# Kernel tuning notes

Hardware: AMD Instinct MI355X
Metric: run time of the kernel (lower is better)

The kernel has to match this reference:

```python
import jax, jax.numpy as jnp
import numpy as np

SQRT_2_OVER_PI = 0.7978845608028654
GELU_COEFF = 0.044715

def _gelu_tanh(v):
    inner = SQRT_2_OVER_PI * (v + GELU_COEFF * v * v * v)
    return 0.5 * v * (1.0 + jnp.tanh(inner))

def setup_inputs() -> dict:
    key = jax.random.key(0)
    k1, k2, k3, k4 = jax.random.split(key, 4)
    M, K, N = 16384, 4096, 4096
    x = jax.random.normal(k1, (M, K), dtype=jnp.float32)
    bound_w = np.sqrt(6.0 / K) / np.sqrt(1.0 + 5.0)  # kaiming_uniform a=sqrt(5)
    weight = jax.random.uniform(k2, (K, N), dtype=jnp.float32, minval=-bound_w, maxval=bound_w)
    bound_b = 1.0 / np.sqrt(K)
    bias = jax.random.uniform(k3, (N,), dtype=jnp.float32, minval=-bound_b, maxval=bound_b)
    subtract = jax.random.normal(k4, (N,), dtype=jnp.float32)
    return {"x": x, "weight": weight, "bias": bias, "subtract": subtract}

def reference(x, weight, bias, subtract):
    # mean_n(xW + b - s) = (x . colsum(W) + sum(b) - sum(s)) / N
    N = weight.shape[1]
    c = weight.sum(axis=1)                       # (K,)
    scale = 1.0 / N
    bias_term = (bias.sum() - subtract.sum()) * scale
    row_scalars = _gelu_tanh(x @ c * scale + bias_term)  # (M,)
    return x + row_scalars[:, None]
```

## Files before the change

kernel.cpp:

```cpp
#include <hip/hip_runtime.h>
#include <math.h>

#define K_DIM 4096
#define N_DIM 4096

typedef float f32x4 __attribute__((ext_vector_type(4)));

__global__ void __launch_bounds__(256) colsum_kernel(const float* __restrict__ W,
                                                     const float* __restrict__ bias,
                                                     const float* __restrict__ subtract,
                                                     float* __restrict__ c,
                                                     float* __restrict__ bterm) {
    const int t = threadIdx.x;
    __shared__ float s[4];
    const int wave = t >> 6, lane = t & 63;

    if (blockIdx.x < K_DIM) {
        const int k = blockIdx.x;
        const f32x4* row = reinterpret_cast<const f32x4*>(W + (size_t)k * N_DIM);
        float acc = 0.f;
#pragma unroll
        for (int i = 0; i < N_DIM / 4 / 256; ++i) {
            f32x4 v = __builtin_nontemporal_load(&row[t + i * 256]);
            acc += (v.x + v.y) + (v.z + v.w);
        }
#pragma unroll
        for (int off = 32; off > 0; off >>= 1) acc += __shfl_down(acc, off, 64);
        if (lane == 0) s[wave] = acc;
        __syncthreads();
        if (t == 0) c[k] = (s[0] + s[1]) + (s[2] + s[3]);
    } else {
        float acc = 0.f;
        for (int i = t; i < N_DIM; i += 256) acc += bias[i] - subtract[i];
#pragma unroll
        for (int off = 32; off > 0; off >>= 1) acc += __shfl_down(acc, off, 64);
        if (lane == 0) s[wave] = acc;
        __syncthreads();
        if (t == 0) bterm[0] = ((s[0] + s[1]) + (s[2] + s[3])) * (1.0f / (float)N_DIM);
    }
}


#define PROCESS(XV, ROFF)                                                        \
    do {                                                                         \
        float a0 = 0.f, a1 = 0.f, a2 = 0.f, a3 = 0.f;                            \
        _Pragma("unroll")                                                        \
        for (int i = 0; i < 16; ++i) {                                           \
            f32x4 cvv = c4[lane + i * 64];                                       \
            a0 += XV[i].x * cvv.x;                                               \
            a1 += XV[i].y * cvv.y;                                               \
            a2 += XV[i].z * cvv.z;                                               \
            a3 += XV[i].w * cvv.w;                                               \
        }                                                                        \
        float acc = (a0 + a1) + (a2 + a3);                                       \
        _Pragma("unroll")                                                        \
        for (int off = 32; off > 0; off >>= 1) acc += __shfl_xor(acc, off, 64);  \
        float d = acc * (1.0f / (float)N_DIM) + bt;                              \
        float inner = 0.7978845608028654f * (d + 0.044715f * d * d * d);         \
        float e  = __expf(2.0f * inner);                                         \
        float g  = 0.5f * d * (1.0f + (1.0f - 2.0f / (e + 1.0f)));               \
        _Pragma("unroll")                                                        \
        for (int i = 0; i < 16; ++i) {                                           \
            f32x4 o = XV[i] + g;                                                 \
            __builtin_nontemporal_store(o, &orow[(size_t)(ROFF) * 1024 + lane + i * 64]); \
        }                                                                        \
    } while (0)

__global__ void __launch_bounds__(256) rowfuse_kernel(const float* __restrict__ x,
                                                      const float* __restrict__ c,
                                                      const float* __restrict__ bterm,
                                                      float* __restrict__ out) {
    const int t = threadIdx.x;
    const int wave = t >> 6, lane = t & 63;
    const size_t w = (size_t)blockIdx.x * 4 + wave;

    const f32x4* c4 = reinterpret_cast<const f32x4*>(c);
    const f32x4* xr = reinterpret_cast<const f32x4*>(x) + w * 4 * (K_DIM / 4);
    f32x4* orow     = reinterpret_cast<f32x4*>(out)     + w * 4 * (K_DIM / 4);
    const float bt = bterm[0];

    f32x4 xa[16], xb[16];
#pragma unroll
    for (int i = 0; i < 16; ++i) xa[i] = __builtin_nontemporal_load(&xr[lane + i * 64]);

#pragma unroll
    for (int i = 0; i < 16; ++i) xb[i] = __builtin_nontemporal_load(&xr[1024 + lane + i * 64]);
    PROCESS(xa, 0);

#pragma unroll
    for (int i = 0; i < 16; ++i) xa[i] = __builtin_nontemporal_load(&xr[2048 + lane + i * 64]);
    PROCESS(xb, 1);

#pragma unroll
    for (int i = 0; i < 16; ++i) xb[i] = __builtin_nontemporal_load(&xr[3072 + lane + i * 64]);
    PROCESS(xa, 2);

    PROCESS(xb, 3);
}

extern "C" void kernel_launch(void* const* d_in, const int* in_sizes, int n_in,
                              void* d_out, int out_size, void* d_ws, size_t ws_size,
                              hipStream_t stream) {
    const float* x        = (const float*)d_in[0];
    const float* W        = (const float*)d_in[1];
    const float* bias     = (const float*)d_in[2];
    const float* subtract = (const float*)d_in[3];
    float* out = (float*)d_out;

    float* c     = (float*)d_ws;
    float* bterm = c + K_DIM;

    const int M = in_sizes[0] / K_DIM;

    colsum_kernel<<<K_DIM + 1, 256, 0, stream>>>(W, bias, subtract, c, bterm);
    rowfuse_kernel<<<M / 16, 256, 0, stream>>>(x, c, bterm, out);
}
```

Before: 114.8 us.

## Fuse column-sum and row GELU kernels into one cooperative grid-synced kernel

Replaces the two launches with a single cooperative kernel. Each wave first sums two rows of W into c and preloads its first x row, then the grid synchronizes before each wave processes eight rows of x in a double-buffered pipeline. The aim is to remove the second launch and the gap between kernels, and to overlap the W reduction with the x prefetch. The cost is a grid-wide barrier, plus the requirement that all 256 blocks of 512 threads are co-resident under launch_bounds(512,2) with 32 f32x4 registers per thread.

```diff
diff --git a/kernel.cpp b/kernel.cpp
--- a/kernel.cpp
+++ b/kernel.cpp
@@ -1,4 +1,5 @@
 #include <hip/hip_runtime.h>
+#include <hip/hip_cooperative_groups.h>
 #include <math.h>
 
 #define K_DIM 4096
@@ -6,40 +7,7 @@
 
 typedef float f32x4 __attribute__((ext_vector_type(4)));
 
-__global__ void __launch_bounds__(256) colsum_kernel(const float* __restrict__ W,
-                                                     const float* __restrict__ bias,
-                                                     const float* __restrict__ subtract,
-                                                     float* __restrict__ c,
-                                                     float* __restrict__ bterm) {
-    const int t = threadIdx.x;
-    __shared__ float s[4];
-    const int wave = t >> 6, lane = t & 63;
-
-    if (blockIdx.x < K_DIM) {
-        const int k = blockIdx.x;
-        const f32x4* row = reinterpret_cast<const f32x4*>(W + (size_t)k * N_DIM);
-        float acc = 0.f;
-#pragma unroll
-        for (int i = 0; i < N_DIM / 4 / 256; ++i) {
-            f32x4 v = __builtin_nontemporal_load(&row[t + i * 256]);
-            acc += (v.x + v.y) + (v.z + v.w);
-        }
-#pragma unroll
-        for (int off = 32; off > 0; off >>= 1) acc += __shfl_down(acc, off, 64);
-        if (lane == 0) s[wave] = acc;
-        __syncthreads();
-        if (t == 0) c[k] = (s[0] + s[1]) + (s[2] + s[3]);
-    } else {
-        float acc = 0.f;
-        for (int i = t; i < N_DIM; i += 256) acc += bias[i] - subtract[i];
-#pragma unroll
-        for (int off = 32; off > 0; off >>= 1) acc += __shfl_down(acc, off, 64);
-        if (lane == 0) s[wave] = acc;
-        __syncthreads();
-        if (t == 0) bterm[0] = ((s[0] + s[1]) + (s[2] + s[3])) * (1.0f / (float)N_DIM);
-    }
-}
-
+namespace cg = cooperative_groups;
 
 #define PROCESS(XV, ROFF)                                                        \
     do {                                                                         \
@@ -62,40 +30,78 @@
         _Pragma("unroll")                                                        \
         for (int i = 0; i < 16; ++i) {                                           \
             f32x4 o = XV[i] + g;                                                 \
-            __builtin_nontemporal_store(o, &orow[(size_t)(ROFF) * 1024 + lane + i * 64]); \
+            __builtin_nontemporal_store(o, &o4[(size_t)(ROFF) * 1024 + lane + i * 64]); \
         }                                                                        \
     } while (0)
 
-__global__ void __launch_bounds__(256) rowfuse_kernel(const float* __restrict__ x,
-                                                      const float* __restrict__ c,
-                                                      const float* __restrict__ bterm,
-                                                      float* __restrict__ out) {
+#define LOADB(BUF, R)                                                            \
+    do {                                                                         \
+        _Pragma("unroll")                                                        \
+        for (int i = 0; i < 16; ++i)                                             \
+            BUF[i] = __builtin_nontemporal_load(&x4[(size_t)(R) * 1024 + lane + i * 64]); \
+    } while (0)
+
+__global__ void __launch_bounds__(512, 2) fused_kernel(const float* __restrict__ x,
+                                                       const float* __restrict__ W,
+                                                       const float* __restrict__ bias,
+                                                       const float* __restrict__ subtract,
+                                                       float* __restrict__ c,
+                                                       float* __restrict__ out) {
     const int t = threadIdx.x;
     const int wave = t >> 6, lane = t & 63;
-    const size_t w = (size_t)blockIdx.x * 4 + wave;
+    const int wid = blockIdx.x * 8 + wave;
+    __shared__ float sbt;
 
+    const f32x4* x4 = reinterpret_cast<const f32x4*>(x) + (size_t)wid * 8 * (K_DIM / 4);
+    f32x4*       o4 = reinterpret_cast<f32x4*>(out)     + (size_t)wid * 8 * (K_DIM / 4);
     const f32x4* c4 = reinterpret_cast<const f32x4*>(c);
-    const f32x4* xr = reinterpret_cast<const f32x4*>(x) + w * 4 * (K_DIM / 4);
-    f32x4* orow     = reinterpret_cast<f32x4*>(out)     + w * 4 * (K_DIM / 4);
-    const float bt = bterm[0];
 
     f32x4 xa[16], xb[16];
+
+    LOADB(xa, 0);
+
+#pragma unroll 2
+    for (int rr = 0; rr < 2; ++rr) {
+        const int k = wid * 2 + rr;
+        const f32x4* wr = reinterpret_cast<const f32x4*>(W + (size_t)k * N_DIM);
+        float a0 = 0.f, a1 = 0.f, a2 = 0.f, a3 = 0.f;
 #pragma unroll
-    for (int i = 0; i < 16; ++i) xa[i] = __builtin_nontemporal_load(&xr[lane + i * 64]);
+        for (int i = 0; i < 16; ++i) {
+            f32x4 v = __builtin_nontemporal_load(&wr[lane + i * 64]);
+            a0 += v.x; a1 += v.y; a2 += v.z; a3 += v.w;
+        }
+        float acc = (a0 + a1) + (a2 + a3);
+#pragma unroll
+        for (int off = 32; off > 0; off >>= 1) acc += __shfl_xor(acc, off, 64);
+        if (lane == 0) c[k] = acc;
+    }
 
+    if (wave == 0) {
+        const f32x4* b4 = reinterpret_cast<const f32x4*>(bias);
+        const f32x4* s4 = reinterpret_cast<const f32x4*>(subtract);
+        float acc = 0.f;
 #pragma unroll
-    for (int i = 0; i < 16; ++i) xb[i] = __builtin_nontemporal_load(&xr[1024 + lane + i * 64]);
-    PROCESS(xa, 0);
+        for (int i = 0; i < 16; ++i) {
+            f32x4 bv = b4[lane + i * 64];
+            f32x4 sv = s4[lane + i * 64];
+            acc += (bv.x - sv.x) + (bv.y - sv.y) + (bv.z - sv.z) + (bv.w - sv.w);
+        }
+#pragma unroll
+        for (int off = 32; off > 0; off >>= 1) acc += __shfl_xor(acc, off, 64);
+        if (lane == 0) sbt = acc * (1.0f / (float)N_DIM);
+    }
 
-#pragma unroll
-    for (int i = 0; i < 16; ++i) xa[i] = __builtin_nontemporal_load(&xr[2048 + lane + i * 64]);
-    PROCESS(xb, 1);
+    cg::this_grid().sync();
+    const float bt = sbt;
 
-#pragma unroll
-    for (int i = 0; i < 16; ++i) xb[i] = __builtin_nontemporal_load(&xr[3072 + lane + i * 64]);
-    PROCESS(xa, 2);
-
-    PROCESS(xb, 3);
+    LOADB(xb, 1); PROCESS(xa, 0);
+    LOADB(xa, 2); PROCESS(xb, 1);
+    LOADB(xb, 3); PROCESS(xa, 2);
+    LOADB(xa, 4); PROCESS(xb, 3);
+    LOADB(xb, 5); PROCESS(xa, 4);
+    LOADB(xa, 6); PROCESS(xb, 5);
+    LOADB(xb, 7); PROCESS(xa, 6);
+    PROCESS(xb, 7);
 }
 
 extern "C" void kernel_launch(void* const* d_in, const int* in_sizes, int n_in,
@@ -106,12 +112,13 @@
     const float* bias     = (const float*)d_in[2];
     const float* subtract = (const float*)d_in[3];
     float* out = (float*)d_out;
-
-    float* c     = (float*)d_ws;
-    float* bterm = c + K_DIM;
+    float* c   = (float*)d_ws;
 
     const int M = in_sizes[0] / K_DIM;
+    const int blocks = M / 64;
 
-    colsum_kernel<<<K_DIM + 1, 256, 0, stream>>>(W, bias, subtract, c, bterm);
-    rowfuse_kernel<<<M / 16, 256, 0, stream>>>(x, c, bterm, out);
+    void* args[] = { (void*)&x, (void*)&W, (void*)&bias, (void*)&subtract,
+                     (void*)&c, (void*)&out };
+    hipLaunchCooperativeKernel((const void*)fused_kernel, dim3(blocks), dim3(512),
+                               args, 0, stream);
 }
```

Result: slower. 185.3 us (+61.4%).
